# Kernel optimization log

Hardware: AMD Instinct MI355X
Metric: run time of the kernel (lower is better)

The kernel has to match this reference:

```python
import jax, jax.numpy as jnp
import numpy as np

B, N, D, NH, HID = 64, 197, 768, 8, 3072
LN_EPS = 1e-5

def _ln(x, g, b):
    m = x.mean(-1, keepdims=True)
    v = x.var(-1, keepdims=True)
    return (x - m) / jnp.sqrt(v + LN_EPS) * g + b

def _so8_gate(x, w, bias, scale, eps):
    # x: [B,N,Dg]; eps: [B,N,8 heads,4 planes]. Closed-form SO(8) planar rotations
    # (equivalent to matrix_exp of the 4 sparse 2x2-block generators, composed).
    Bb, Nn, Dg = x.shape
    hd = Dg // 8
    xp = x @ w.T + bias                      # orth_monitor Linear
    xh = xp.reshape(Bb, Nn, 8, hd)           # [B,N,H,hd]
    x8 = xh[..., :8]                         # first 8 channels per head
    ang = eps * scale                        # angles = randn * rotation_scale
    c, s = jnp.cos(ang), jnp.sin(ang)        # [B,N,8,4]
    ev, od = x8[..., 0::2], x8[..., 1::2]    # plane components
    rot8 = jnp.stack([ev * c - od * s, ev * s + od * c], -1).reshape(Bb, Nn, 8, 8)
    rotated = jnp.concatenate([rot8, xh[..., 8:]], -1)
    err = jnp.linalg.norm(rot8 - x8, axis=-1).mean(-1)  # fro norm per head, mean over heads -> [B,N]
    return rotated.reshape(Bb, Nn, Dg) + x, err

def _adapter(x, w, bias, scale, ln_g, ln_b, eps):
    y, err = _so8_gate(x, w, bias, scale, eps)
    return _ln(y, ln_g, ln_b) + x, err

def setup_inputs():
    key = jax.random.key(0)
    ks = jax.random.split(key, 26)
    rn = lambda k, shp, s=0.02: (jax.random.normal(k, shp) * s).astype(jnp.float32)
    z = lambda shp: jnp.zeros(shp, jnp.float32)
    o = lambda shp: jnp.ones(shp, jnp.float32)
    return {
        'x': jax.random.normal(ks[0], (B, N, D), jnp.float32),
        'qkv_w': rn(ks[1], (3 * D, D)), 'qkv_b': z((3 * D,)),
        'proj_w': rn(ks[2], (D, D)), 'proj_b': z((D,)),
        'norm1_g': o((D,)), 'norm1_b': z((D,)),
        'norm2_g': o((D,)), 'norm2_b': z((D,)),
        'orth_w_a': rn(ks[3], (D, D)), 'orth_b_a': z((D,)),
        'scale_a': o((1,)), 'ln_g_a': o((D,)), 'ln_b_a': z((D,)),
        'orth_w_m': rn(ks[4], (HID, HID)), 'orth_b_m': z((HID,)),
        'scale_m': o((1,)), 'ln_g_m': o((HID,)), 'ln_b_m': z((HID,)),
        'fc1_w': rn(ks[5], (HID, D)), 'fc1_b': z((HID,)),
        'fc2_w': rn(ks[6], (D, HID)), 'fc2_b': z((D,)),
        'eps_a': jax.random.normal(ks[7], (B, N, 8, 4), jnp.float32),
        'eps_m': jax.random.normal(ks[8], (B, N, 8, 4), jnp.float32),
    }

def reference(x, qkv_w, qkv_b, proj_w, proj_b, norm1_g, norm1_b, norm2_g, norm2_b,
              orth_w_a, orth_b_a, scale_a, ln_g_a, ln_b_a,
              orth_w_m, orth_b_m, scale_m, ln_g_m, ln_b_m,
              fc1_w, fc1_b, fc2_w, fc2_b, eps_a, eps_m):
    hd = D // NH
    # attention branch
    x1 = _ln(x, norm1_g, norm1_b)
    qkv = (x1 @ qkv_w.T + qkv_b).reshape(B, N, 3, NH, hd).transpose(2, 0, 3, 1, 4)
    q, k, v = qkv[0], qkv[1], qkv[2]
    attn = jax.nn.softmax(jnp.einsum('bhqd,bhkd->bhqk', q, k) * hd ** -0.5, -1)
    ctx = jnp.einsum('bhqk,bhkd->bhqd', attn, v).transpose(0, 2, 1, 3).reshape(B, N, D)
    ctx = ctx @ proj_w.T + proj_b
    xa, e1 = _adapter(ctx, orth_w_a, orth_b_a, scale_a, ln_g_a, ln_b_a, eps_a)
    x = x + xa
    # mlp branch with SO(8) adapter on hidden
    x2 = _ln(x, norm2_g, norm2_b)
    h = jax.nn.gelu(x2 @ fc1_w.T + fc1_b, approximate=False)
    h, e2 = _adapter(h, orth_w_m, orth_b_m, scale_m, ln_g_m, ln_b_m, eps_m)
    xm = h @ fc2_w.T + fc2_b
    x = x + xm
    return x, e1 + e2
```

## Files before the change

kernel.cpp:

```cpp
#include <hip/hip_runtime.h>
#include <hip/hip_bf16.h>
#include <math.h>
#include <type_traits>

#define MROWS (64*197)
#define DMODEL 768
#define DHID   3072

typedef __hip_bfloat16 bf16;
using bf16x8 = __attribute__((ext_vector_type(8))) short;
using f32x4  = __attribute__((ext_vector_type(4))) float;

__device__ __forceinline__ float b2f(bf16 v) { return __bfloat162float(v); }
__device__ __forceinline__ float tof(float v) { return v; }
__device__ __forceinline__ float tof(bf16 v) { return __bfloat162float(v); }
__device__ __forceinline__ short f2bs(float f) {
    bf16 h = __float2bfloat16(f);
    return *reinterpret_cast<short*>(&h);
}
__device__ __forceinline__ float gelu_exact(float v) {
    return 0.5f * v * (1.0f + erff(v * 0.70710678118654752f));
}
__device__ __forceinline__ void st1(bf16* p, float v) { *p = __float2bfloat16(v); }
__device__ __forceinline__ void st1(float* p, float v) { *p = v; }

__device__ __forceinline__ void gl_lds16(const short* g, short* l) {
    __builtin_amdgcn_global_load_lds(
        (const __attribute__((address_space(1))) void*)g,
        (__attribute__((address_space(3))) void*)l, 16, 0, 0);
}

__global__ __launch_bounds__(256) void cvt_w_kernel(const float* __restrict__ src,
        short* __restrict__ dst, int n4) {
    int i = blockIdx.x * 256 + threadIdx.x;
    if (i < n4) {
        float4 v = ((const float4*)src)[i];
        short4 h = make_short4(f2bs(v.x), f2bs(v.y), f2bs(v.z), f2bs(v.w));
        ((short4*)dst)[i] = h;
    }
}

template<typename TIN>
__global__ __launch_bounds__(256) void ln_kernel(const TIN* __restrict__ in,
        const float* __restrict__ g, const float* __restrict__ b,
        bf16* __restrict__ out, int Dg) {
    int row = blockIdx.x;
    const TIN* xr = in + (size_t)row * Dg;
    bf16* yr = out + (size_t)row * Dg;
    float s = 0.f, s2 = 0.f;
    for (int c = threadIdx.x; c < Dg; c += 256) { float v = tof(xr[c]); s += v; s2 += v * v; }
    __shared__ float r1[4], r2[4];
    for (int off = 32; off; off >>= 1) { s += __shfl_down(s, off, 64); s2 += __shfl_down(s2, off, 64); }
    if ((threadIdx.x & 63) == 0) { r1[threadIdx.x >> 6] = s; r2[threadIdx.x >> 6] = s2; }
    __syncthreads();
    s  = r1[0] + r1[1] + r1[2] + r1[3];
    s2 = r2[0] + r2[1] + r2[2] + r2[3];
    float mean = s / Dg;
    float var  = s2 / Dg - mean * mean;
    float rstd = rsqrtf(var + 1e-5f);
    for (int c = threadIdx.x; c < Dg; c += 256)
        yr[c] = __float2bfloat16((tof(xr[c]) - mean) * rstd * g[c] + b[c]);
}

template<int MODE, typename TC, typename TB>
__global__ __launch_bounds__(256) void gemm_mfma(const short* __restrict__ A,
        const TB* __restrict__ W, const float* __restrict__ bias,
        const bf16* __restrict__ resid, TC* __restrict__ C,
        int Mr, int Nc, int Kc)
{
    __shared__ short Abuf[128 * 32];
    __shared__ short Bbuf[128 * 32];
    const int tid  = threadIdx.x;
    const int lane = tid & 63, wave = tid >> 6;
    const int wm = wave & 1, wn = wave >> 1;
    const int quad = lane >> 4, l16 = lane & 15;
    const int m0 = blockIdx.y * 128, n0 = blockIdx.x * 128;

    f32x4 acc[4][4];
#pragma unroll
    for (int i = 0; i < 4; ++i)
#pragma unroll
        for (int j = 0; j < 4; ++j) acc[i][j] = (f32x4){0.f, 0.f, 0.f, 0.f};

    const int brow = tid >> 3;
    const int bk   = (tid & 7) * 4;

    for (int k0 = 0; k0 < Kc; k0 += 32) {
        if constexpr (std::is_same<TB, float>::value) {
            float4 wv[4];
#pragma unroll
            for (int s = 0; s < 4; ++s)
                wv[s] = *(const float4*)(W + (size_t)(n0 + s * 32 + brow) * Kc + k0 + bk);
            __syncthreads();
#pragma unroll
            for (int q = 0; q < 2; ++q) {
                int c = q * 256 + tid;
                int rowA = m0 + (c >> 2);
                if (rowA > Mr - 1) rowA = Mr - 1;
                gl_lds16(A + (size_t)rowA * Kc + k0 + (c & 3) * 8, Abuf + c * 8);
            }
#pragma unroll
            for (int s = 0; s < 4; ++s) {
                short4 h;
                h.x = f2bs(wv[s].x); h.y = f2bs(wv[s].y);
                h.z = f2bs(wv[s].z); h.w = f2bs(wv[s].w);
                *(short4*)(Bbuf + (s * 32 + brow) * 32 + bk) = h;
            }
            __syncthreads();
        } else {
            __syncthreads();
#pragma unroll
            for (int q = 0; q < 2; ++q) {
                int c = q * 256 + tid;
                int rowA = m0 + (c >> 2);
                if (rowA > Mr - 1) rowA = Mr - 1;
                gl_lds16(A + (size_t)rowA * Kc + k0 + (c & 3) * 8, Abuf + c * 8);
            }
#pragma unroll
            for (int q = 0; q < 2; ++q) {
                int c = q * 256 + tid;
                gl_lds16((const short*)W + (size_t)(n0 + (c >> 2)) * Kc + k0 + (c & 3) * 8,
                         Bbuf + c * 8);
            }
            __syncthreads();
        }
        bf16x8 fa[4], fb[4];
#pragma unroll
        for (int i = 0; i < 4; ++i)
            fa[i] = *(const bf16x8*)(Abuf + (wm * 64 + i * 16 + l16) * 32 + quad * 8);
#pragma unroll
        for (int j = 0; j < 4; ++j)
            fb[j] = *(const bf16x8*)(Bbuf + (wn * 64 + j * 16 + l16) * 32 + quad * 8);
#pragma unroll
        for (int i = 0; i < 4; ++i)
#pragma unroll
            for (int j = 0; j < 4; ++j)
                acc[i][j] = __builtin_amdgcn_mfma_f32_16x16x32_bf16(fa[i], fb[j], acc[i][j], 0, 0, 0);
    }

#pragma unroll
    for (int i = 0; i < 4; ++i)
#pragma unroll
        for (int r = 0; r < 4; ++r) {
            int row = m0 + wm * 64 + i * 16 + quad * 4 + r;
            if (row >= Mr) continue;
#pragma unroll
            for (int j = 0; j < 4; ++j) {
                int col = n0 + wn * 64 + j * 16 + l16;
                float v = acc[i][j][r] + bias[col];
                if (MODE == 1) v = gelu_exact(v);
                if (MODE == 2) v += b2f(resid[(size_t)row * Nc + col]);
                st1(C + (size_t)row * Nc + col, v);
            }
        }
}

__global__ __launch_bounds__(256) void attn_mfma(const bf16* __restrict__ qkv,
        bf16* __restrict__ ctx) {
    const int NS = 197;
    const int KST = 104;
    const int VST = 232;
    __shared__ short Kbuf[224 * KST];
    __shared__ short Vt[96 * VST];
    __shared__ short Pbuf[4][16 * VST];
    const int b = blockIdx.x >> 3, h = blockIdx.x & 7;
    const short* base = (const short*)qkv + (size_t)b * NS * 2304 + h * 96;
    const int tid = threadIdx.x;

    for (int c = tid; c < NS * 12; c += 256) {
        int key = c / 12, dc = c % 12;
        bf16x8 v = *(const bf16x8*)(base + (size_t)key * 2304 + 768 + dc * 8);
        *(bf16x8*)(Kbuf + key * KST + dc * 8) = v;
    }
    for (int c = tid; c < 27 * 12; c += 256) {
        int key = NS + c / 12, dc = c % 12;
        *(bf16x8*)(Kbuf + key * KST + dc * 8) = (bf16x8){0, 0, 0, 0, 0, 0, 0, 0};
    }
    for (int c = tid; c < NS * 12; c += 256) {
        int key = c / 12, dc = c % 12;
        bf16x8 v = *(const bf16x8*)(base + (size_t)key * 2304 + 1536 + dc * 8);
#pragma unroll
        for (int j = 0; j < 8; ++j) Vt[(dc * 8 + j) * VST + key] = v[j];
    }
    for (int c = tid; c < 96 * 27; c += 256) {
        int d = c / 27, key = NS + c % 27;
        Vt[d * VST + key] = 0;
    }
    __syncthreads();

    const int wave = tid >> 6, lane = tid & 63;
    const int quad = lane >> 4, l16 = lane & 15;
    short* P = &Pbuf[wave][0];

    for (int qt = wave; qt < 13; qt += 4) {
        int qrow = qt * 16 + l16; if (qrow > NS - 1) qrow = NS - 1;
        bf16x8 fq[3];
#pragma unroll
        for (int kc = 0; kc < 3; ++kc)
            fq[kc] = *(const bf16x8*)(base + (size_t)qrow * 2304 + kc * 32 + quad * 8);
        f32x4 s[14];
#pragma unroll
        for (int nt = 0; nt < 14; ++nt) {
            s[nt] = (f32x4){0.f, 0.f, 0.f, 0.f};
#pragma unroll
            for (int kc = 0; kc < 3; ++kc) {
                bf16x8 fk = *(const bf16x8*)(Kbuf + (nt * 16 + l16) * KST + kc * 32 + quad * 8);
                s[nt] = __builtin_amdgcn_mfma_f32_16x16x32_bf16(fq[kc], fk, s[nt], 0, 0, 0);
            }
        }
        const float sc = 0.10206207261596577f;
        float mx[4] = {-1e30f, -1e30f, -1e30f, -1e30f};
#pragma unroll
        for (int nt = 0; nt < 14; ++nt) {
            bool valid = nt * 16 + l16 < NS;
#pragma unroll
            for (int r = 0; r < 4; ++r) {
                float v = s[nt][r] * sc;
                s[nt][r] = v;
                if (valid) mx[r] = fmaxf(mx[r], v);
            }
        }
#pragma unroll
        for (int m = 1; m < 16; m <<= 1)
#pragma unroll
            for (int r = 0; r < 4; ++r) mx[r] = fmaxf(mx[r], __shfl_xor(mx[r], m, 64));
        float l[4] = {0.f, 0.f, 0.f, 0.f};
#pragma unroll
        for (int nt = 0; nt < 14; ++nt) {
            bool valid = nt * 16 + l16 < NS;
#pragma unroll
            for (int r = 0; r < 4; ++r) {
                float e = valid ? __expf(s[nt][r] - mx[r]) : 0.f;
                l[r] += e;
                P[(quad * 4 + r) * VST + nt * 16 + l16] = f2bs(e);
            }
        }
#pragma unroll
        for (int m = 1; m < 16; m <<= 1)
#pragma unroll
            for (int r = 0; r < 4; ++r) l[r] += __shfl_xor(l[r], m, 64);
        __asm__ volatile("s_waitcnt lgkmcnt(0)" ::: "memory");
        f32x4 o[6];
#pragma unroll
        for (int nt = 0; nt < 6; ++nt) o[nt] = (f32x4){0.f, 0.f, 0.f, 0.f};
#pragma unroll
        for (int kc = 0; kc < 7; ++kc) {
            bf16x8 fp = *(const bf16x8*)(P + l16 * VST + kc * 32 + quad * 8);
#pragma unroll
            for (int nt = 0; nt < 6; ++nt) {
                bf16x8 fv = *(const bf16x8*)(Vt + (nt * 16 + l16) * VST + kc * 32 + quad * 8);
                o[nt] = __builtin_amdgcn_mfma_f32_16x16x32_bf16(fp, fv, o[nt], 0, 0, 0);
            }
        }
        float inv[4];
#pragma unroll
        for (int r = 0; r < 4; ++r) inv[r] = 1.f / l[r];
#pragma unroll
        for (int r = 0; r < 4; ++r) {
            int q = qt * 16 + quad * 4 + r;
            if (q >= NS) continue;
            bf16* orow = ctx + ((size_t)(b * NS + q)) * 768 + h * 96;
#pragma unroll
            for (int nt = 0; nt < 6; ++nt)
                orow[nt * 16 + l16] = __float2bfloat16(o[nt][r] * inv[r]);
        }
    }
}

template<bool OUTER, bool FINAL>
__global__ __launch_bounds__(256) void adapter_finish(
        const bf16* __restrict__ xp, const bf16* __restrict__ xin,
        const float* __restrict__ xouter, const float* __restrict__ eps,
        const float* __restrict__ scale_p, const float* __restrict__ g,
        const float* __restrict__ bta, bf16* __restrict__ out,
        float* __restrict__ e_acc, float* __restrict__ e_out, int Dg)
{
    extern __shared__ float smem[];
    float* y = smem;
    float* diff2 = smem + Dg;
    float* red = diff2 + 64;
    float* r1 = red + 8;
    float* r2 = red + 12;
    int row = blockIdx.x;
    int hd = Dg >> 3;
    const bf16* xpr = xp + (size_t)row * Dg;
    const bf16* xir = xin + (size_t)row * Dg;
    int tid = threadIdx.x;
    if (tid < 64) {
        int hh = tid >> 3, i = tid & 7, p = i >> 1;
        float ang = eps[((size_t)row * 8 + hh) * 4 + p] * scale_p[0];
        float c = cosf(ang), sn = sinf(ang);
        int base = hh * hd;
        float ev = b2f(xpr[base + 2 * p]), od = b2f(xpr[base + 2 * p + 1]);
        float r = (i & 1) ? (ev * sn + od * c) : (ev * c - od * sn);
        float d = r - b2f(xpr[base + i]);
        diff2[tid] = d * d;
        y[base + i] = r + b2f(xir[base + i]);
    }
    for (int c0 = tid; c0 < Dg; c0 += 256) {
        if ((c0 % hd) >= 8) y[c0] = b2f(xpr[c0]) + b2f(xir[c0]);
    }
    __syncthreads();
    if (tid < 8) {
        float t = 0.f;
#pragma unroll
        for (int i = 0; i < 8; ++i) t += diff2[tid * 8 + i];
        red[tid] = sqrtf(t);
    }
    float s = 0.f, s2 = 0.f;
    for (int c0 = tid; c0 < Dg; c0 += 256) { float v = y[c0]; s += v; s2 += v * v; }
    for (int off = 32; off; off >>= 1) { s += __shfl_down(s, off, 64); s2 += __shfl_down(s2, off, 64); }
    if ((tid & 63) == 0) { r1[tid >> 6] = s; r2[tid >> 6] = s2; }
    __syncthreads();
    s  = r1[0] + r1[1] + r1[2] + r1[3];
    s2 = r2[0] + r2[1] + r2[2] + r2[3];
    float mean = s / Dg;
    float var  = s2 / Dg - mean * mean;
    float rstd = rsqrtf(var + 1e-5f);
    if (tid == 0) {
        float e = (red[0] + red[1] + red[2] + red[3] + red[4] + red[5] + red[6] + red[7]) * 0.125f;
        if (FINAL) e_out[row] = e_acc[row] + e;
        else       e_acc[row] = e;
    }
    bf16* outr = out + (size_t)row * Dg;
    const float* xo = OUTER ? (xouter + (size_t)row * Dg) : nullptr;
    for (int c0 = tid; c0 < Dg; c0 += 256) {
        float v = (y[c0] - mean) * rstd * g[c0] + bta[c0] + b2f(xir[c0]);
        if (OUTER) v += xo[c0];
        outr[c0] = __float2bfloat16(v);
    }
}

extern "C" void kernel_launch(void* const* d_in, const int* in_sizes, int n_in,
                              void* d_out, int out_size, void* d_ws, size_t ws_size,
                              hipStream_t stream) {
    (void)in_sizes; (void)n_in; (void)out_size;
    const int M = MROWS;
    const size_t S_D = (size_t)M * DMODEL;
    const size_t S_H = (size_t)M * DHID;

    const float* x      = (const float*)d_in[0];
    const float* qkv_w  = (const float*)d_in[1];
    const float* qkv_b  = (const float*)d_in[2];
    const float* proj_w = (const float*)d_in[3];
    const float* proj_b = (const float*)d_in[4];
    const float* n1g    = (const float*)d_in[5];
    const float* n1b    = (const float*)d_in[6];
    const float* n2g    = (const float*)d_in[7];
    const float* n2b    = (const float*)d_in[8];
    const float* wa     = (const float*)d_in[9];
    const float* ba     = (const float*)d_in[10];
    const float* sca    = (const float*)d_in[11];
    const float* lga    = (const float*)d_in[12];
    const float* lba    = (const float*)d_in[13];
    const float* wm     = (const float*)d_in[14];
    const float* bm     = (const float*)d_in[15];
    const float* scm    = (const float*)d_in[16];
    const float* lgm    = (const float*)d_in[17];
    const float* lbm    = (const float*)d_in[18];
    const float* f1w    = (const float*)d_in[19];
    const float* f1b    = (const float*)d_in[20];
    const float* f2w    = (const float*)d_in[21];
    const float* f2b    = (const float*)d_in[22];
    const float* eps_a  = (const float*)d_in[23];
    const float* eps_m  = (const float*)d_in[24];

    float* out_x = (float*)d_out;
    float* out_e = out_x + S_D;

    bf16* R1 = (bf16*)d_ws;
    bf16* R2 = R1 + S_H;
    bf16* R3 = R2 + S_H;
    float* E = (float*)(R3 + S_D);

    const size_t n_qkv = (size_t)2304 * 768, n_proj = (size_t)768 * 768,
                 n_wa = (size_t)768 * 768, n_wm = (size_t)3072 * 3072,
                 n_f1 = (size_t)3072 * 768, n_f2 = (size_t)768 * 3072;
    const size_t base_bytes = (2 * S_H + S_D) * 2 + (size_t)M * 4;
    const size_t w_elems = n_qkv + n_proj + n_wa + n_wm + n_f1 + n_f2;
    const bool cache_w = ws_size >= base_bytes + w_elems * 2;

    short* WB    = (short*)((char*)d_ws + base_bytes);
    short* wb_qkv = WB;
    short* wb_proj = wb_qkv + n_qkv;
    short* wb_wa  = wb_proj + n_proj;
    short* wb_wm  = wb_wa + n_wa;
    short* wb_f1  = wb_wm + n_wm;
    short* wb_f2  = wb_f1 + n_f1;

    const int GY = (M + 127) / 128;

    if (cache_w) {
        cvt_w_kernel<<<(int)(n_qkv / 4 + 255) / 256, 256, 0, stream>>>(qkv_w, wb_qkv, (int)(n_qkv / 4));
        cvt_w_kernel<<<(int)(n_proj / 4 + 255) / 256, 256, 0, stream>>>(proj_w, wb_proj, (int)(n_proj / 4));
        cvt_w_kernel<<<(int)(n_wa / 4 + 255) / 256, 256, 0, stream>>>(wa, wb_wa, (int)(n_wa / 4));
        cvt_w_kernel<<<(int)(n_wm / 4 + 255) / 256, 256, 0, stream>>>(wm, wb_wm, (int)(n_wm / 4));
        cvt_w_kernel<<<(int)(n_f1 / 4 + 255) / 256, 256, 0, stream>>>(f1w, wb_f1, (int)(n_f1 / 4));
        cvt_w_kernel<<<(int)(n_f2 / 4 + 255) / 256, 256, 0, stream>>>(f2w, wb_f2, (int)(n_f2 / 4));
    }

    ln_kernel<float><<<M, 256, 0, stream>>>(x, n1g, n1b, R1, DMODEL);
    if (cache_w) {
        gemm_mfma<0, bf16, short><<<dim3(2304 / 128, GY), 256, 0, stream>>>(
            (const short*)R1, wb_qkv, qkv_b, nullptr, R2, M, 2304, DMODEL);
        attn_mfma<<<64 * 8, 256, 0, stream>>>(R2, R1);
        gemm_mfma<0, bf16, short><<<dim3(DMODEL / 128, GY), 256, 0, stream>>>(
            (const short*)R1, wb_proj, proj_b, nullptr, R2, M, DMODEL, DMODEL);
        gemm_mfma<0, bf16, short><<<dim3(DMODEL / 128, GY), 256, 0, stream>>>(
            (const short*)R2, wb_wa, ba, nullptr, R1, M, DMODEL, DMODEL);
        adapter_finish<true, false><<<M, 256, (DMODEL + 80) * sizeof(float), stream>>>(
            R1, R2, x, eps_a, sca, lga, lba, R3, E, nullptr, DMODEL);
        ln_kernel<bf16><<<M, 256, 0, stream>>>(R3, n2g, n2b, R2, DMODEL);
        gemm_mfma<1, bf16, short><<<dim3(DHID / 128, GY), 256, 0, stream>>>(
            (const short*)R2, wb_f1, f1b, nullptr, R1, M, DHID, DMODEL);
        gemm_mfma<0, bf16, short><<<dim3(DHID / 128, GY), 256, 0, stream>>>(
            (const short*)R1, wb_wm, bm, nullptr, R2, M, DHID, DHID);
        adapter_finish<false, true><<<M, 256, (DHID + 80) * sizeof(float), stream>>>(
            R2, R1, nullptr, eps_m, scm, lgm, lbm, R1, E, out_e, DHID);
        gemm_mfma<2, float, short><<<dim3(DMODEL / 128, GY), 256, 0, stream>>>(
            (const short*)R1, wb_f2, f2b, R3, out_x, M, DMODEL, DHID);
    } else {
        gemm_mfma<0, bf16, float><<<dim3(2304 / 128, GY), 256, 0, stream>>>(
            (const short*)R1, qkv_w, qkv_b, nullptr, R2, M, 2304, DMODEL);
        attn_mfma<<<64 * 8, 256, 0, stream>>>(R2, R1);
        gemm_mfma<0, bf16, float><<<dim3(DMODEL / 128, GY), 256, 0, stream>>>(
            (const short*)R1, proj_w, proj_b, nullptr, R2, M, DMODEL, DMODEL);
        gemm_mfma<0, bf16, float><<<dim3(DMODEL / 128, GY), 256, 0, stream>>>(
            (const short*)R2, wa, ba, nullptr, R1, M, DMODEL, DMODEL);
        adapter_finish<true, false><<<M, 256, (DMODEL + 80) * sizeof(float), stream>>>(
            R1, R2, x, eps_a, sca, lga, lba, R3, E, nullptr, DMODEL);
        ln_kernel<bf16><<<M, 256, 0, stream>>>(R3, n2g, n2b, R2, DMODEL);
        gemm_mfma<1, bf16, float><<<dim3(DHID / 128, GY), 256, 0, stream>>>(
            (const short*)R2, f1w, f1b, nullptr, R1, M, DHID, DMODEL);
        gemm_mfma<0, bf16, float><<<dim3(DHID / 128, GY), 256, 0, stream>>>(
            (const short*)R1, wm, bm, nullptr, R2, M, DHID, DHID);
        adapter_finish<false, true><<<M, 256, (DHID + 80) * sizeof(float), stream>>>(
            R2, R1, nullptr, eps_m, scm, lgm, lbm, R1, E, out_e, DHID);
        gemm_mfma<2, float, float><<<dim3(DMODEL / 128, GY), 256, 0, stream>>>(
            (const short*)R1, f2w, f2b, R3, out_x, M, DMODEL, DHID);
    }
}
```

Before: 1.100 ms.

## Fuse LN2 into adapter, merge weight casts, swizzle K64 GEMM, vectorize row kernels

The bf16-weight GEMM now stages K=64 tiles with an XOR-swizzled LDS layout, which halves the number of barriers per tile and is meant to avoid LDS bank conflicts. The six weight-conversion launches become one kernel. The second LayerNorm is fused into the attention adapter epilogue, so one full read and write pass over the activations is dropped. The LN and adapter kernels use vectorized float4 and bf16x8 loads. The trade-off is more LDS per block (32KB), which may lower occupancy, and higher register and code complexity in the adapter.

Result: faster. 911.2 us (-17.1%).

```diff
diff --git a/kernel.cpp b/kernel.cpp
--- a/kernel.cpp
+++ b/kernel.cpp
@@ -1,7 +1,6 @@
 #include <hip/hip_runtime.h>
 #include <hip/hip_bf16.h>
 #include <math.h>
-#include <type_traits>
 
 #define MROWS (64*197)
 #define DMODEL 768
@@ -12,11 +11,20 @@
 using f32x4  = __attribute__((ext_vector_type(4))) float;
 
 __device__ __forceinline__ float b2f(bf16 v) { return __bfloat162float(v); }
-__device__ __forceinline__ float tof(float v) { return v; }
-__device__ __forceinline__ float tof(bf16 v) { return __bfloat162float(v); }
 __device__ __forceinline__ short f2bs(float f) {
     bf16 h = __float2bfloat16(f);
     return *reinterpret_cast<short*>(&h);
+}
+__device__ __forceinline__ void b8f(bf16x8 v, float* f) {
+#pragma unroll
+    for (int j = 0; j < 8; ++j)
+        f[j] = __uint_as_float(((unsigned int)(unsigned short)v[j]) << 16);
+}
+__device__ __forceinline__ bf16x8 f8b(const float* f) {
+    bf16x8 r;
+#pragma unroll
+    for (int j = 0; j < 8; ++j) r[j] = f2bs(f[j]);
+    return r;
 }
 __device__ __forceinline__ float gelu_exact(float v) {
     return 0.5f * v * (1.0f + erff(v * 0.70710678118654752f));
@@ -30,25 +38,38 @@
         (__attribute__((address_space(3))) void*)l, 16, 0, 0);
 }
 
-__global__ __launch_bounds__(256) void cvt_w_kernel(const float* __restrict__ src,
-        short* __restrict__ dst, int n4) {
+__global__ __launch_bounds__(256) void cvt_all_kernel(
+        const float* __restrict__ s0, const float* __restrict__ s1,
+        const float* __restrict__ s2, const float* __restrict__ s3,
+        const float* __restrict__ s4, const float* __restrict__ s5,
+        short* __restrict__ dst) {
+    const int b0 = 442368, b1 = 589824, b2 = 737280,
+              b3 = 3096576, b4 = 3686400, b5 = 4276224;
     int i = blockIdx.x * 256 + threadIdx.x;
-    if (i < n4) {
-        float4 v = ((const float4*)src)[i];
-        short4 h = make_short4(f2bs(v.x), f2bs(v.y), f2bs(v.z), f2bs(v.w));
-        ((short4*)dst)[i] = h;
-    }
-}
-
-template<typename TIN>
-__global__ __launch_bounds__(256) void ln_kernel(const TIN* __restrict__ in,
+    if (i >= b5) return;
+    const float* src; int off;
+    if      (i < b0) { src = s0; off = i; }
+    else if (i < b1) { src = s1; off = i - b0; }
+    else if (i < b2) { src = s2; off = i - b1; }
+    else if (i < b3) { src = s3; off = i - b2; }
+    else if (i < b4) { src = s4; off = i - b3; }
+    else             { src = s5; off = i - b4; }
+    float4 v = ((const float4*)src)[off];
+    ((short4*)dst)[i] = make_short4(f2bs(v.x), f2bs(v.y), f2bs(v.z), f2bs(v.w));
+}
+
+__global__ __launch_bounds__(256) void ln1_kernel(const float* __restrict__ in,
         const float* __restrict__ g, const float* __restrict__ b,
         bf16* __restrict__ out, int Dg) {
     int row = blockIdx.x;
-    const TIN* xr = in + (size_t)row * Dg;
-    bf16* yr = out + (size_t)row * Dg;
+    int n4 = Dg >> 2;
+    const float4* xr = (const float4*)(in + (size_t)row * Dg);
     float s = 0.f, s2 = 0.f;
-    for (int c = threadIdx.x; c < Dg; c += 256) { float v = tof(xr[c]); s += v; s2 += v * v; }
+    for (int c = threadIdx.x; c < n4; c += 256) {
+        float4 v = xr[c];
+        s += v.x + v.y + v.z + v.w;
+        s2 += v.x * v.x + v.y * v.y + v.z * v.z + v.w * v.w;
+    }
     __shared__ float r1[4], r2[4];
     for (int off = 32; off; off >>= 1) { s += __shfl_down(s, off, 64); s2 += __shfl_down(s2, off, 64); }
     if ((threadIdx.x & 63) == 0) { r1[threadIdx.x >> 6] = s; r2[threadIdx.x >> 6] = s2; }
@@ -56,15 +77,99 @@
     s  = r1[0] + r1[1] + r1[2] + r1[3];
     s2 = r2[0] + r2[1] + r2[2] + r2[3];
     float mean = s / Dg;
-    float var  = s2 / Dg - mean * mean;
-    float rstd = rsqrtf(var + 1e-5f);
-    for (int c = threadIdx.x; c < Dg; c += 256)
-        yr[c] = __float2bfloat16((tof(xr[c]) - mean) * rstd * g[c] + b[c]);
-}
-
-template<int MODE, typename TC, typename TB>
-__global__ __launch_bounds__(256) void gemm_mfma(const short* __restrict__ A,
-        const TB* __restrict__ W, const float* __restrict__ bias,
+    float rstd = rsqrtf(s2 / Dg - mean * mean + 1e-5f);
+    short4* yr = (short4*)(out + (size_t)row * Dg);
+    const float4* g4 = (const float4*)g;
+    const float4* b4 = (const float4*)b;
+    for (int c = threadIdx.x; c < n4; c += 256) {
+        float4 v = xr[c], gg = g4[c], bb = b4[c];
+        yr[c] = make_short4(f2bs((v.x - mean) * rstd * gg.x + bb.x),
+                            f2bs((v.y - mean) * rstd * gg.y + bb.y),
+                            f2bs((v.z - mean) * rstd * gg.z + bb.z),
+                            f2bs((v.w - mean) * rstd * gg.w + bb.w));
+    }
+}
+
+template<int MODE, typename TC>
+__global__ __launch_bounds__(256) void gemm_bf(const short* __restrict__ A,
+        const short* __restrict__ W, const float* __restrict__ bias,
+        const bf16* __restrict__ resid, TC* __restrict__ C,
+        int Mr, int Nc, int Kc)
+{
+    __shared__ short Abuf[128 * 64];
+    __shared__ short Bbuf[128 * 64];
+    const int tid  = threadIdx.x;
+    const int lane = tid & 63, wave = tid >> 6;
+    const int wm = wave & 1, wn = wave >> 1;
+    const int quad = lane >> 4, l16 = lane & 15;
+    const int m0 = blockIdx.y * 128, n0 = blockIdx.x * 128;
+
+    f32x4 acc[4][4];
+#pragma unroll
+    for (int i = 0; i < 4; ++i)
+#pragma unroll
+        for (int j = 0; j < 4; ++j) acc[i][j] = (f32x4){0.f, 0.f, 0.f, 0.f};
+
+    for (int k0 = 0; k0 < Kc; k0 += 64) {
+        __syncthreads();
+#pragma unroll
+        for (int q = 0; q < 4; ++q) {
+            int c = q * 256 + tid;
+            int row = c >> 3;
+            int j = (c & 7) ^ (row & 7);
+            int rowA = m0 + row;
+            if (rowA > Mr - 1) rowA = Mr - 1;
+            gl_lds16(A + (size_t)rowA * Kc + k0 + j * 8, Abuf + c * 8);
+        }
+#pragma unroll
+        for (int q = 0; q < 4; ++q) {
+            int c = q * 256 + tid;
+            int row = c >> 3;
+            int j = (c & 7) ^ (row & 7);
+            gl_lds16(W + (size_t)(n0 + row) * Kc + k0 + j * 8, Bbuf + c * 8);
+        }
+        __syncthreads();
+#pragma unroll
+        for (int t = 0; t < 2; ++t) {
+            bf16x8 fa[4], fb[4];
+#pragma unroll
+            for (int i = 0; i < 4; ++i) {
+                int r = wm * 64 + i * 16 + l16;
+                fa[i] = *(const bf16x8*)(Abuf + r * 64 + (((t * 4 + quad) ^ (r & 7)) << 3));
+            }
+#pragma unroll
+            for (int j = 0; j < 4; ++j) {
+                int r = wn * 64 + j * 16 + l16;
+                fb[j] = *(const bf16x8*)(Bbuf + r * 64 + (((t * 4 + quad) ^ (r & 7)) << 3));
+            }
+#pragma unroll
+            for (int i = 0; i < 4; ++i)
+#pragma unroll
+                for (int j = 0; j < 4; ++j)
+                    acc[i][j] = __builtin_amdgcn_mfma_f32_16x16x32_bf16(fa[i], fb[j], acc[i][j], 0, 0, 0);
+        }
+    }
+
+#pragma unroll
+    for (int i = 0; i < 4; ++i)
+#pragma unroll
+        for (int r = 0; r < 4; ++r) {
+            int row = m0 + wm * 64 + i * 16 + quad * 4 + r;
+            if (row >= Mr) continue;
+#pragma unroll
+            for (int j = 0; j < 4; ++j) {
+                int col = n0 + wn * 64 + j * 16 + l16;
+                float v = acc[i][j][r] + bias[col];
+                if (MODE == 1) v = gelu_exact(v);
+                if (MODE == 2) v += b2f(resid[(size_t)row * Nc + col]);
+                st1(C + (size_t)row * Nc + col, v);
+            }
+        }
+}
+
+template<int MODE, typename TC>
+__global__ __launch_bounds__(256) void gemm_f32b(const short* __restrict__ A,
+        const float* __restrict__ W, const float* __restrict__ bias,
         const bf16* __restrict__ resid, TC* __restrict__ C,
         int Mr, int Nc, int Kc)
 {
@@ -75,55 +180,32 @@
     const int wm = wave & 1, wn = wave >> 1;
     const int quad = lane >> 4, l16 = lane & 15;
     const int m0 = blockIdx.y * 128, n0 = blockIdx.x * 128;
-
     f32x4 acc[4][4];
 #pragma unroll
     for (int i = 0; i < 4; ++i)
 #pragma unroll
         for (int j = 0; j < 4; ++j) acc[i][j] = (f32x4){0.f, 0.f, 0.f, 0.f};
-
     const int brow = tid >> 3;
     const int bk   = (tid & 7) * 4;
-
     for (int k0 = 0; k0 < Kc; k0 += 32) {
-        if constexpr (std::is_same<TB, float>::value) {
-            float4 wv[4];
-#pragma unroll
-            for (int s = 0; s < 4; ++s)
-                wv[s] = *(const float4*)(W + (size_t)(n0 + s * 32 + brow) * Kc + k0 + bk);
-            __syncthreads();
-#pragma unroll
-            for (int q = 0; q < 2; ++q) {
-                int c = q * 256 + tid;
-                int rowA = m0 + (c >> 2);
-                if (rowA > Mr - 1) rowA = Mr - 1;
-                gl_lds16(A + (size_t)rowA * Kc + k0 + (c & 3) * 8, Abuf + c * 8);
-            }
-#pragma unroll
-            for (int s = 0; s < 4; ++s) {
-                short4 h;
-                h.x = f2bs(wv[s].x); h.y = f2bs(wv[s].y);
-                h.z = f2bs(wv[s].z); h.w = f2bs(wv[s].w);
-                *(short4*)(Bbuf + (s * 32 + brow) * 32 + bk) = h;
-            }
-            __syncthreads();
-        } else {
-            __syncthreads();
-#pragma unroll
-            for (int q = 0; q < 2; ++q) {
-                int c = q * 256 + tid;
-                int rowA = m0 + (c >> 2);
-                if (rowA > Mr - 1) rowA = Mr - 1;
-                gl_lds16(A + (size_t)rowA * Kc + k0 + (c & 3) * 8, Abuf + c * 8);
-            }
-#pragma unroll
-            for (int q = 0; q < 2; ++q) {
-                int c = q * 256 + tid;
-                gl_lds16((const short*)W + (size_t)(n0 + (c >> 2)) * Kc + k0 + (c & 3) * 8,
-                         Bbuf + c * 8);
-            }
-            __syncthreads();
-        }
+        float4 wv[4];
+#pragma unroll
+        for (int s = 0; s < 4; ++s)
+            wv[s] = *(const float4*)(W + (size_t)(n0 + s * 32 + brow) * Kc + k0 + bk);
+        __syncthreads();
+#pragma unroll
+        for (int q = 0; q < 2; ++q) {
+            int c = q * 256 + tid;
+            int rowA = m0 + (c >> 2);
+            if (rowA > Mr - 1) rowA = Mr - 1;
+            gl_lds16(A + (size_t)rowA * Kc + k0 + (c & 3) * 8, Abuf + c * 8);
+        }
+#pragma unroll
+        for (int s = 0; s < 4; ++s) {
+            short4 h = make_short4(f2bs(wv[s].x), f2bs(wv[s].y), f2bs(wv[s].z), f2bs(wv[s].w));
+            *(short4*)(Bbuf + (s * 32 + brow) * 32 + bk) = h;
+        }
+        __syncthreads();
         bf16x8 fa[4], fb[4];
 #pragma unroll
         for (int i = 0; i < 4; ++i)
@@ -137,7 +219,6 @@
             for (int j = 0; j < 4; ++j)
                 acc[i][j] = __builtin_amdgcn_mfma_f32_16x16x32_bf16(fa[i], fb[j], acc[i][j], 0, 0, 0);
     }
-
 #pragma unroll
     for (int i = 0; i < 4; ++i)
 #pragma unroll
@@ -267,13 +348,15 @@
     }
 }
 
-template<bool OUTER, bool FINAL>
+template<bool OUTER, bool FINAL, bool FLN2>
 __global__ __launch_bounds__(256) void adapter_finish(
         const bf16* __restrict__ xp, const bf16* __restrict__ xin,
         const float* __restrict__ xouter, const float* __restrict__ eps,
         const float* __restrict__ scale_p, const float* __restrict__ g,
         const float* __restrict__ bta, bf16* __restrict__ out,
-        float* __restrict__ e_acc, float* __restrict__ e_out, int Dg)
+        float* __restrict__ e_acc, float* __restrict__ e_out,
+        const float* __restrict__ g2, const float* __restrict__ b2,
+        bf16* __restrict__ out2, int Dg)
 {
     extern __shared__ float smem[];
     float* y = smem;
@@ -283,6 +366,8 @@
     float* r2 = red + 12;
     int row = blockIdx.x;
     int hd = Dg >> 3;
+    int hd8 = hd >> 3;
+    int n8 = Dg >> 3;
     const bf16* xpr = xp + (size_t)row * Dg;
     const bf16* xir = xin + (size_t)row * Dg;
     int tid = threadIdx.x;
@@ -297,8 +382,13 @@
         diff2[tid] = d * d;
         y[base + i] = r + b2f(xir[base + i]);
     }
-    for (int c0 = tid; c0 < Dg; c0 += 256) {
-        if ((c0 % hd) >= 8) y[c0] = b2f(xpr[c0]) + b2f(xir[c0]);
+    for (int c8 = tid; c8 < n8; c8 += 256) {
+        if (c8 % hd8 == 0) continue;
+        float a[8], bvx[8];
+        b8f(*(const bf16x8*)(xpr + c8 * 8), a);
+        b8f(*(const bf16x8*)(xir + c8 * 8), bvx);
+#pragma unroll
+        for (int j = 0; j < 8; ++j) y[c8 * 8 + j] = a[j] + bvx[j];
     }
     __syncthreads();
     if (tid < 8) {
@@ -308,26 +398,73 @@
         red[tid] = sqrtf(t);
     }
     float s = 0.f, s2 = 0.f;
-    for (int c0 = tid; c0 < Dg; c0 += 256) { float v = y[c0]; s += v; s2 += v * v; }
+    for (int c = tid; c < Dg; c += 256) { float v = y[c]; s += v; s2 += v * v; }
     for (int off = 32; off; off >>= 1) { s += __shfl_down(s, off, 64); s2 += __shfl_down(s2, off, 64); }
     if ((tid & 63) == 0) { r1[tid >> 6] = s; r2[tid >> 6] = s2; }
     __syncthreads();
     s  = r1[0] + r1[1] + r1[2] + r1[3];
     s2 = r2[0] + r2[1] + r2[2] + r2[3];
     float mean = s / Dg;
-    float var  = s2 / Dg - mean * mean;
-    float rstd = rsqrtf(var + 1e-5f);
+    float rstd = rsqrtf(s2 / Dg - mean * mean + 1e-5f);
     if (tid == 0) {
         float e = (red[0] + red[1] + red[2] + red[3] + red[4] + red[5] + red[6] + red[7]) * 0.125f;
         if (FINAL) e_out[row] = e_acc[row] + e;
         else       e_acc[row] = e;
     }
     bf16* outr = out + (size_t)row * Dg;
-    const float* xo = OUTER ? (xouter + (size_t)row * Dg) : nullptr;
-    for (int c0 = tid; c0 < Dg; c0 += 256) {
-        float v = (y[c0] - mean) * rstd * g[c0] + bta[c0] + b2f(xir[c0]);
-        if (OUTER) v += xo[c0];
-        outr[c0] = __float2bfloat16(v);
+    const float4* g4 = (const float4*)g;
+    const float4* bt4 = (const float4*)bta;
+    const float4* xo4 = OUTER ? (const float4*)(xouter + (size_t)row * Dg) : nullptr;
+    float sB = 0.f, sB2 = 0.f;
+    for (int c8 = tid; c8 < n8; c8 += 256) {
+        float xi[8];
+        b8f(*(const bf16x8*)(xir + c8 * 8), xi);
+        float4 gg0 = g4[c8 * 2], gg1 = g4[c8 * 2 + 1];
+        float4 bb0 = bt4[c8 * 2], bb1 = bt4[c8 * 2 + 1];
+        float gv[8] = {gg0.x, gg0.y, gg0.z, gg0.w, gg1.x, gg1.y, gg1.z, gg1.w};
+        float bv[8] = {bb0.x, bb0.y, bb0.z, bb0.w, bb1.x, bb1.y, bb1.z, bb1.w};
+        float vv[8];
+#pragma unroll
+        for (int j = 0; j < 8; ++j)
+            vv[j] = (y[c8 * 8 + j] - mean) * rstd * gv[j] + bv[j] + xi[j];
+        if (OUTER) {
+            float4 o0 = xo4[c8 * 2], o1 = xo4[c8 * 2 + 1];
+            float ov[8] = {o0.x, o0.y, o0.z, o0.w, o1.x, o1.y, o1.z, o1.w};
+#pragma unroll
+            for (int j = 0; j < 8; ++j) vv[j] += ov[j];
+        }
+        *(bf16x8*)(outr + c8 * 8) = f8b(vv);
+        if (FLN2) {
+#pragma unroll
+            for (int j = 0; j < 8; ++j) {
+                y[c8 * 8 + j] = vv[j];
+                sB += vv[j]; sB2 += vv[j] * vv[j];
+            }
+        }
+    }
+    if (FLN2) {
+        __syncthreads();
+        for (int off = 32; off; off >>= 1) { sB += __shfl_down(sB, off, 64); sB2 += __shfl_down(sB2, off, 64); }
+        if ((tid & 63) == 0) { r1[tid >> 6] = sB; r2[tid >> 6] = sB2; }
+        __syncthreads();
+        sB  = r1[0] + r1[1] + r1[2] + r1[3];
+        sB2 = r2[0] + r2[1] + r2[2] + r2[3];
+        float mean2 = sB / Dg;
+        float rstd2 = rsqrtf(sB2 / Dg - mean2 * mean2 + 1e-5f);
+        bf16* o2r = out2 + (size_t)row * Dg;
+        const float4* g24 = (const float4*)g2;
+        const float4* b24 = (const float4*)b2;
+        for (int c8 = tid; c8 < n8; c8 += 256) {
+            float4 gg0 = g24[c8 * 2], gg1 = g24[c8 * 2 + 1];
+            float4 bb0 = b24[c8 * 2], bb1 = b24[c8 * 2 + 1];
+            float gv[8] = {gg0.x, gg0.y, gg0.z, gg0.w, gg1.x, gg1.y, gg1.z, gg1.w};
+            float bv[8] = {bb0.x, bb0.y, bb0.z, bb0.w, bb1.x, bb1.y, bb1.z, bb1.w};
+            float vv[8];
+#pragma unroll
+            for (int j = 0; j < 8; ++j)
+                vv[j] = (y[c8 * 8 + j] - mean2) * rstd2 * gv[j] + bv[j];
+            *(bf16x8*)(o2r + c8 * 8) = f8b(vv);
+        }
     }
 }
 
@@ -389,54 +526,48 @@
     short* wb_f2  = wb_f1 + n_f1;
 
     const int GY = (M + 127) / 128;
+    const size_t lds_a = (DMODEL + 96) * sizeof(float);
+    const size_t lds_m = (DHID + 96) * sizeof(float);
 
     if (cache_w) {
-        cvt_w_kernel<<<(int)(n_qkv / 4 + 255) / 256, 256, 0, stream>>>(qkv_w, wb_qkv, (int)(n_qkv / 4));
-        cvt_w_kernel<<<(int)(n_proj / 4 + 255) / 256, 256, 0, stream>>>(proj_w, wb_proj, (int)(n_proj / 4));
-        cvt_w_kernel<<<(int)(n_wa / 4 + 255) / 256, 256, 0, stream>>>(wa, wb_wa, (int)(n_wa / 4));
-        cvt_w_kernel<<<(int)(n_wm / 4 + 255) / 256, 256, 0, stream>>>(wm, wb_wm, (int)(n_wm / 4));
-        cvt_w_kernel<<<(int)(n_f1 / 4 + 255) / 256, 256, 0, stream>>>(f1w, wb_f1, (int)(n_f1 / 4));
-        cvt_w_kernel<<<(int)(n_f2 / 4 + 255) / 256, 256, 0, stream>>>(f2w, wb_f2, (int)(n_f2 / 4));
-    }
-
-    ln_kernel<float><<<M, 256, 0, stream>>>(x, n1g, n1b, R1, DMODEL);
-    if (cache_w) {
-        gemm_mfma<0, bf16, short><<<dim3(2304 / 128, GY), 256, 0, stream>>>(
+        cvt_all_kernel<<<(4276224 + 255) / 256, 256, 0, stream>>>(
+            qkv_w, proj_w, wa, wm, f1w, f2w, WB);
+        ln1_kernel<<<M, 256, 0, stream>>>(x, n1g, n1b, R1, DMODEL);
+        gemm_bf<0, bf16><<<dim3(2304 / 128, GY), 256, 0, stream>>>(
             (const short*)R1, wb_qkv, qkv_b, nullptr, R2, M, 2304, DMODEL);
         attn_mfma<<<64 * 8, 256, 0, stream>>>(R2, R1);
-        gemm_mfma<0, bf16, short><<<dim3(DMODEL / 128, GY), 256, 0, stream>>>(
+        gemm_bf<0, bf16><<<dim3(DMODEL / 128, GY), 256, 0, stream>>>(
             (const short*)R1, wb_proj, proj_b, nullptr, R2, M, DMODEL, DMODEL);
-        gemm_mfma<0, bf16, short><<<dim3(DMODEL / 128, GY), 256, 0, stream>>>(
+        gemm_bf<0, bf16><<<dim3(DMODEL / 128, GY), 256, 0, stream>>>(
             (const short*)R2, wb_wa, ba, nullptr, R1, M, DMODEL, DMODEL);
-        adapter_finish<true, false><<<M, 256, (DMODEL + 80) * sizeof(float), stream>>>(
-            R1, R2, x, eps_a, sca, lga, lba, R3, E, nullptr, DMODEL);
-        ln_kernel<bf16><<<M, 256, 0, stream>>>(R3, n2g, n2b, R2, DMODEL);
-        gemm_mfma<1, bf16, short><<<dim3(DHID / 128, GY), 256, 0, stream>>>(
+        adapter_finish<true, false, true><<<M, 256, lds_a, stream>>>(
+            R1, R2, x, eps_a, sca, lga, lba, R3, E, nullptr, n2g, n2b, R2, DMODEL);
+        gemm_bf<1, bf16><<<dim3(DHID / 128, GY), 256, 0, stream>>>(
             (const short*)R2, wb_f1, f1b, nullptr, R1, M, DHID, DMODEL);
-        gemm_mfma<0, bf16, short><<<dim3(DHID / 128, GY), 256, 0, stream>>>(
+        gemm_bf<0, bf16><<<dim3(DHID / 128, GY), 256, 0, stream>>>(
             (const short*)R1, wb_wm, bm, nullptr, R2, M, DHID, DHID);
-        adapter_finish<false, true><<<M, 256, (DHID + 80) * sizeof(float), stream>>>(
-            R2, R1, nullptr, eps_m, scm, lgm, lbm, R1, E, out_e, DHID);
-        gemm_mfma<2, float, short><<<dim3(DMODEL / 128, GY), 256, 0, stream>>>(
+        adapter_finish<false, true, false><<<M, 256, lds_m, stream>>>(
+            R2, R1, nullptr, eps_m, scm, lgm, lbm, R1, E, out_e, nullptr, nullptr, nullptr, DHID);
+        gemm_bf<2, float><<<dim3(DMODEL / 128, GY), 256, 0, stream>>>(
             (const short*)R1, wb_f2, f2b, R3, out_x, M, DMODEL, DHID);
     } else {
-        gemm_mfma<0, bf16, float><<<dim3(2304 / 128, GY), 256, 0, stream>>>(
+        ln1_kernel<<<M, 256, 0, stream>>>(x, n1g, n1b, R1, DMODEL);
+        gemm_f32b<0, bf16><<<dim3(2304 / 128, GY), 256, 0, stream>>>(
             (const short*)R1, qkv_w, qkv_b, nullptr, R2, M, 2304, DMODEL);
         attn_mfma<<<64 * 8, 256, 0, stream>>>(R2, R1);
-        gemm_mfma<0, bf16, float><<<dim3(DMODEL / 128, GY), 256, 0, stream>>>(
+        gemm_f32b<0, bf16><<<dim3(DMODEL / 128, GY), 256, 0, stream>>>(
             (const short*)R1, proj_w, proj_b, nullptr, R2, M, DMODEL, DMODEL);
-        gemm_mfma<0, bf16, float><<<dim3(DMODEL / 128, GY), 256, 0, stream>>>(
+        gemm_f32b<0, bf16><<<dim3(DMODEL / 128, GY), 256, 0, stream>>>(
             (const short*)R2, wa, ba, nullptr, R1, M, DMODEL, DMODEL);
-        adapter_finish<true, false><<<M, 256, (DMODEL + 80) * sizeof(float), stream>>>(
-            R1, R2, x, eps_a, sca, lga, lba, R3, E, nullptr, DMODEL);
-        ln_kernel<bf16><<<M, 256, 0, stream>>>(R3, n2g, n2b, R2, DMODEL);
-        gemm_mfma<1, bf16, float><<<dim3(DHID / 128, GY), 256, 0, stream>>>(
+        adapter_finish<true, false, true><<<M, 256, lds_a, stream>>>(
+            R1, R2, x, eps_a, sca, lga, lba, R3, E, nullptr, n2g, n2b, R2, DMODEL);
+        gemm_f32b<1, bf16><<<dim3(DHID / 128, GY), 256, 0, stream>>>(
             (const short*)R2, f1w, f1b, nullptr, R1, M, DHID, DMODEL);
-        gemm_mfma<0, bf16, float><<<dim3(DHID / 128, GY), 256, 0, stream>>>(
+        gemm_f32b<0, bf16><<<dim3(DHID / 128, GY), 256, 0, stream>>>(
             (const short*)R1, wm, bm, nullptr, R2, M, DHID, DHID);
-        adapter_finish<false, true><<<M, 256, (DHID + 80) * sizeof(float), stream>>>(
-            R2, R1, nullptr, eps_m, scm, lgm, lbm, R1, E, out_e, DHID);
-        gemm_mfma<2, float, float><<<dim3(DMODEL / 128, GY), 256, 0, stream>>>(
+        adapter_finish<false, true, false><<<M, 256, lds_m, stream>>>(
+            R2, R1, nullptr, eps_m, scm, lgm, lbm, R1, E, out_e, nullptr, nullptr, nullptr, DHID);
+        gemm_f32b<2, float><<<dim3(DMODEL / 128, GY), 256, 0, stream>>>(
             (const short*)R1, f2w, f2b, R3, out_x, M, DMODEL, DHID);
     }
 }
```
